# Performance work log

Measured on AMD Instinct MI355X. Metric: run time of the kernel, lower is better.

## Reference

```python
import jax, jax.numpy as jnp
import numpy as np

EMBED_DIM = 768
NUM_HEADS = 12
HEAD_DIM = EMBED_DIM // NUM_HEADS
SCALE = HEAD_DIM ** -0.5


def setup_inputs() -> dict:
    key = jax.random.key(0)
    k1, k2, k3, k4, k5 = jax.random.split(key, 5)
    B, T = 8, 1024
    hidden_states = jax.random.normal(k1, (B, T, EMBED_DIM), dtype=jnp.float32)
    init = 0.02
    qkv_w = jax.random.normal(k2, (EMBED_DIM, 3 * EMBED_DIM), dtype=jnp.float32) * init
    qkv_b = jnp.zeros((3 * EMBED_DIM,), dtype=jnp.float32)
    proj_w = jax.random.normal(k3, (EMBED_DIM, EMBED_DIM), dtype=jnp.float32) * init
    proj_b = jnp.zeros((EMBED_DIM,), dtype=jnp.float32)
    return {
        "hidden_states": hidden_states,
        "qkv_w": qkv_w,
        "qkv_b": qkv_b,
        "proj_w": proj_w,
        "proj_b": proj_b,
    }


def reference(hidden_states, qkv_w, qkv_b, proj_w, proj_b):
    B, T, C = hidden_states.shape
    # fused QKV projection
    mixed = hidden_states @ qkv_w + qkv_b            # [B, T, 3C]
    mixed = mixed.reshape(B, T, 3, NUM_HEADS, HEAD_DIM)
    mixed = jnp.transpose(mixed, (2, 0, 3, 1, 4))    # [3, B, H, T, D]
    q, k, v = mixed[0], mixed[1], mixed[2]
    # scaled dot-product attention (dropout is identity in eval)
    scores = jnp.einsum("bhqd,bhkd->bhqk", q, k) * SCALE
    probs = jax.nn.softmax(scores, axis=-1)
    ctx = jnp.einsum("bhqk,bhkd->bhqd", probs, v)    # [B, H, T, D]
    ctx = jnp.transpose(ctx, (0, 2, 1, 3)).reshape(B, T, C)
    out = ctx @ proj_w + proj_b
    return out
```

## Files before the change

kernel.cpp:

```cpp
#include <hip/hip_runtime.h>

#define EMBED 768
#define NHEAD 12
#define HDIM 64
#define BATCH 8
#define SEQ 1024
#define ROWS (BATCH*SEQ)
#define QKVN (3*EMBED)
#define ATTN_SCALE 0.125f

typedef short s16x8 __attribute__((ext_vector_type(8)));
typedef short s16x4 __attribute__((ext_vector_type(4)));
typedef float f32x4 __attribute__((ext_vector_type(4)));

__device__ __forceinline__ float bf2f(unsigned short u) {
    union { unsigned int i; float f; } v; v.i = ((unsigned int)u) << 16; return v.f;
}
__device__ __forceinline__ unsigned short f2bf(float f) {
    unsigned int i = __builtin_bit_cast(unsigned int, f);
    i += 0x7FFFu + ((i >> 16) & 1u);
    return (unsigned short)(i >> 16);
}

__device__ __forceinline__ void async16(short* lds, const unsigned short* g) {
    __builtin_amdgcn_global_load_lds(
        (const __attribute__((address_space(1))) unsigned int*)g,
        (__attribute__((address_space(3))) unsigned int*)lds,
        16, 0, 0);
}

__device__ __forceinline__ f32x4 mfma16(s16x4 a, s16x4 b, f32x4 c) {
#if __has_builtin(__builtin_amdgcn_mfma_f32_16x16x16bf16_1k)
    return __builtin_amdgcn_mfma_f32_16x16x16bf16_1k(a, b, c, 0, 0, 0);
#else
    asm volatile("v_mfma_f32_16x16x16_bf16 %0, %1, %2, %0" : "+v"(c) : "v"(a), "v"(b));
    return c;
#endif
}

__global__ __launch_bounds__(256) void prep_k(
    const float* __restrict__ qkv_w, unsigned short* __restrict__ WqkvT,
    const float* __restrict__ proj_w, unsigned short* __restrict__ WprojT,
    const float* __restrict__ hidden, unsigned short* __restrict__ hiddenBf)
{
    __shared__ float tile[64][65];
    int blk = blockIdx.x;
    int t = threadIdx.x;
    if (blk < 576) {
        const float* in; unsigned short* outp; int K, N, tx, ty;
        if (blk < 432) { in = qkv_w; outp = WqkvT; K = EMBED; N = QKVN; tx = blk % 36; ty = blk / 36; }
        else { int b2 = blk - 432; in = proj_w; outp = WprojT; K = EMBED; N = EMBED; tx = b2 % 12; ty = b2 / 12; }
        int n0 = tx * 64, k0 = ty * 64;
        int c = t & 63, r0 = t >> 6;
        #pragma unroll
        for (int i = 0; i < 16; i++) {
            int r = r0 * 16 + i;
            tile[r][c] = in[(long long)(k0 + r) * N + n0 + c];
        }
        __syncthreads();
        #pragma unroll
        for (int i = 0; i < 16; i++) {
            int nr = r0 * 16 + i;
            outp[(long long)(n0 + nr) * K + k0 + c] = f2bf(tile[c][nr]);
        }
    } else {
        int tid = (blk - 576) * 256 + t;
        int base = tid * 8;
        float4 f0 = *(const float4*)&hidden[base];
        float4 f1 = *(const float4*)&hidden[base + 4];
        s16x8 a;
        a[0] = (short)f2bf(f0.x); a[1] = (short)f2bf(f0.y);
        a[2] = (short)f2bf(f0.z); a[3] = (short)f2bf(f0.w);
        a[4] = (short)f2bf(f1.x); a[5] = (short)f2bf(f1.y);
        a[6] = (short)f2bf(f1.z); a[7] = (short)f2bf(f1.w);
        *(s16x8*)&hiddenBf[base] = a;
    }
}

template <int OUT_F32>
__global__ __launch_bounds__(256) void gemm128(
    const unsigned short* __restrict__ A,
    const unsigned short* __restrict__ Bt,
    const float* __restrict__ bias,
    void* __restrict__ Cv,
    int M, int N, int K)
{
    __shared__ short As[128 * 32];
    __shared__ short Bs[128 * 32];
    int t = threadIdx.x, lane = t & 63, w = t >> 6;
    int quad = lane >> 4, low = lane & 15;
    int m0 = blockIdx.x * 128, n0 = blockIdx.y * 128;
    int wm = (w & 1) * 64, wn = (w >> 1) * 64;

    int ci0 = w * 128 + lane;
    int r0 = ci0 >> 2, c0 = (ci0 & 3) ^ ((r0 >> 1) & 3);
    int ci1 = ci0 + 64;
    int r1 = ci1 >> 2, c1 = (ci1 & 3) ^ ((r1 >> 1) & 3);
    const unsigned short* pa0 = A + (long long)(m0 + r0) * K + c0 * 8;
    const unsigned short* pa1 = A + (long long)(m0 + r1) * K + c1 * 8;
    const unsigned short* pb0 = Bt + (long long)(n0 + r0) * K + c0 * 8;
    const unsigned short* pb1 = Bt + (long long)(n0 + r1) * K + c1 * 8;
    short* la0 = As + (w * 128) * 8;
    short* la1 = As + (w * 128 + 64) * 8;
    short* lb0 = Bs + (w * 128) * 8;
    short* lb1 = Bs + (w * 128 + 64) * 8;

    f32x4 acc[4][4] = {};
    for (int k0 = 0; k0 < K; k0 += 32) {
        __syncthreads();
        async16(la0, pa0 + k0);
        async16(la1, pa1 + k0);
        async16(lb0, pb0 + k0);
        async16(lb1, pb1 + k0);
        __syncthreads();
        s16x8 af[4], bfr[4];
        #pragma unroll
        for (int i = 0; i < 4; i++) {
            int ra = wm + i * 16 + low;
            af[i] = *(const s16x8*)&As[ra * 32 + ((quad ^ ((ra >> 1) & 3)) * 8)];
            int rb = wn + i * 16 + low;
            bfr[i] = *(const s16x8*)&Bs[rb * 32 + ((quad ^ ((rb >> 1) & 3)) * 8)];
        }
        #pragma unroll
        for (int i = 0; i < 4; i++)
            #pragma unroll
            for (int j = 0; j < 4; j++)
                acc[i][j] = __builtin_amdgcn_mfma_f32_16x16x32_bf16(af[i], bfr[j], acc[i][j], 0, 0, 0);
    }
    #pragma unroll
    for (int i = 0; i < 4; i++)
        #pragma unroll
        for (int j = 0; j < 4; j++)
            #pragma unroll
            for (int r = 0; r < 4; r++) {
                int m = m0 + wm + i * 16 + quad * 4 + r;
                int n = n0 + wn + j * 16 + low;
                float v = acc[i][j][r] + bias[n];
                if (OUT_F32) ((float*)Cv)[(long long)m * N + n] = v;
                else ((unsigned short*)Cv)[(long long)m * N + n] = f2bf(v);
            }
}

__global__ __launch_bounds__(256) void attn_k(
    const unsigned short* __restrict__ mixed,
    unsigned short* __restrict__ ctx)
{
    __shared__ short Ks[64 * 64];
    __shared__ short Vt[64 * 68];
    int blk = blockIdx.x;
    int bh = blk % 96;
    int qc = blk / 96;
    int b = bh / NHEAD, h = bh - b * NHEAD;
    int t = threadIdx.x;
    int lane = t & 63, w = t >> 6;
    int quad = lane >> 4, low = lane & 15;
    long long rowbase = (long long)b * SEQ;
    int q0 = qc * 128 + w * 32;
    int hoff = h * HDIM;

    s16x8 qf[2][2];
    #pragma unroll
    for (int qh = 0; qh < 2; qh++) {
        long long r = (rowbase + q0 + qh * 16 + low) * QKVN + hoff;
        qf[qh][0] = *(const s16x8*)&mixed[r + quad * 8];
        qf[qh][1] = *(const s16x8*)&mixed[r + 32 + quad * 8];
    }

    int s0 = w * 128 + lane;
    int kr0 = s0 >> 3, kc0 = s0 & 7;
    int kg = kc0 ^ (kr0 & 7);
    const unsigned short* pk0 = mixed + (rowbase + kr0) * QKVN + EMBED + hoff + kg * 8;
    const unsigned short* pk1 = mixed + (rowbase + kr0 + 8) * QKVN + EMBED + hoff + kg * 8;
    short* lk0 = Ks + (w * 128) * 8;
    short* lk1 = Ks + (w * 128 + 64) * 8;

    int dblk = t & 15, rq = t >> 4;
    const unsigned short* pv = mixed + (rowbase + rq * 4) * QKVN + 2 * EMBED + hoff + dblk * 4;

    f32x4 o[2][4] = {};
    float lsum[2] = {0.f, 0.f};

    for (int kv0 = 0; kv0 < SEQ; kv0 += 64) {
        long long koff = (long long)kv0 * QKVN;
        __syncthreads();
        async16(lk0, pk0 + koff);
        async16(lk1, pk1 + koff);
        s16x4 v0 = *(const s16x4*)&pv[koff];
        s16x4 v1 = *(const s16x4*)&pv[koff + QKVN];
        s16x4 v2 = *(const s16x4*)&pv[koff + 2 * QKVN];
        s16x4 v3 = *(const s16x4*)&pv[koff + 3 * QKVN];
        #pragma unroll
        for (int k = 0; k < 4; k++) {
            s16x4 wv;
            wv[0] = v0[k]; wv[1] = v1[k]; wv[2] = v2[k]; wv[3] = v3[k];
            *(s16x4*)&Vt[(dblk * 4 + k) * 68 + rq * 4] = wv;
        }
        __syncthreads();

        f32x4 sT[2][4] = {};
        __builtin_amdgcn_s_setprio(1);
        #pragma unroll
        for (int n = 0; n < 4; n++) {
            int rr = n * 16 + low;
            int key = low & 7;
            s16x8 kf0 = *(const s16x8*)&Ks[rr * 64 + ((quad ^ key) * 8)];
            s16x8 kf1 = *(const s16x8*)&Ks[rr * 64 + (((quad + 4) ^ key) * 8)];
            sT[0][n] = __builtin_amdgcn_mfma_f32_16x16x32_bf16(kf0, qf[0][0], sT[0][n], 0, 0, 0);
            sT[0][n] = __builtin_amdgcn_mfma_f32_16x16x32_bf16(kf1, qf[0][1], sT[0][n], 0, 0, 0);
            sT[1][n] = __builtin_amdgcn_mfma_f32_16x16x32_bf16(kf0, qf[1][0], sT[1][n], 0, 0, 0);
            sT[1][n] = __builtin_amdgcn_mfma_f32_16x16x32_bf16(kf1, qf[1][1], sT[1][n], 0, 0, 0);
        }
        __builtin_amdgcn_s_setprio(0);

        s16x4 pf[2][4];
        #pragma unroll
        for (int qh = 0; qh < 2; qh++)
            #pragma unroll
            for (int n = 0; n < 4; n++) {
                float e0 = __expf(sT[qh][n][0] * ATTN_SCALE);
                float e1 = __expf(sT[qh][n][1] * ATTN_SCALE);
                float e2 = __expf(sT[qh][n][2] * ATTN_SCALE);
                float e3 = __expf(sT[qh][n][3] * ATTN_SCALE);
                lsum[qh] += (e0 + e1) + (e2 + e3);
                unsigned int w0, w1;
                asm("v_cvt_pk_bf16_f32 %0, %1, %2" : "=v"(w0) : "v"(e0), "v"(e1));
                asm("v_cvt_pk_bf16_f32 %0, %1, %2" : "=v"(w1) : "v"(e2), "v"(e3));
                union { unsigned int u[2]; s16x4 v; } pu;
                pu.u[0] = w0; pu.u[1] = w1;
                pf[qh][n] = pu.v;
            }

        __builtin_amdgcn_s_setprio(1);
        #pragma unroll
        for (int nt = 0; nt < 4; nt++) {
            int drow = nt * 16 + low;
            #pragma unroll
            for (int n = 0; n < 4; n++) {
                s16x4 vf = *(const s16x4*)&Vt[drow * 68 + n * 16 + quad * 4];
                o[0][nt] = mfma16(pf[0][n], vf, o[0][nt]);
                o[1][nt] = mfma16(pf[1][n], vf, o[1][nt]);
            }
        }
        __builtin_amdgcn_s_setprio(0);
    }

    #pragma unroll
    for (int qh = 0; qh < 2; qh++) {
        lsum[qh] += __shfl_xor(lsum[qh], 16, 64);
        lsum[qh] += __shfl_xor(lsum[qh], 32, 64);
    }
    #pragma unroll
    for (int qh = 0; qh < 2; qh++)
        #pragma unroll
        for (int r = 0; r < 4; r++) {
            float inv = 1.0f / __shfl(lsum[qh], quad * 4 + r, 64);
            int q = q0 + qh * 16 + quad * 4 + r;
            #pragma unroll
            for (int nt = 0; nt < 4; nt++)
                ctx[(rowbase + q) * EMBED + hoff + nt * 16 + low] =
                    f2bf(o[qh][nt][r] * inv);
        }
}

extern "C" void kernel_launch(void* const* d_in, const int* in_sizes, int n_in,
                              void* d_out, int out_size, void* d_ws, size_t ws_size,
                              hipStream_t stream) {
    const float* hidden = (const float*)d_in[0];
    const float* qkv_w  = (const float*)d_in[1];
    const float* qkv_b  = (const float*)d_in[2];
    const float* proj_w = (const float*)d_in[3];
    const float* proj_b = (const float*)d_in[4];
    float* out = (float*)d_out;

    char* ws = (char*)d_ws;
    unsigned short* hiddenBf = (unsigned short*)ws;
    unsigned short* ctx      = (unsigned short*)ws;
    unsigned short* WqkvT    = (unsigned short*)(ws + 12582912);
    unsigned short* WprojT   = (unsigned short*)(ws + 16121856);
    unsigned short* mixed    = (unsigned short*)(ws + 17301504);

    prep_k<<<dim3(3648), 256, 0, stream>>>(qkv_w, WqkvT, proj_w, WprojT, hidden, hiddenBf);
    gemm128<0><<<dim3(ROWS / 128, QKVN / 128), 256, 0, stream>>>(
        hiddenBf, WqkvT, qkv_b, mixed, ROWS, QKVN, EMBED);
    attn_k<<<dim3(96 * 8), 256, 0, stream>>>(mixed, ctx);
    gemm128<1><<<dim3(ROWS / 128, EMBED / 128), 256, 0, stream>>>(
        ctx, WprojT, proj_b, out, ROWS, EMBED, EMBED);
}
```

Baseline: 198.5 us.

## Double-buffer K/V tiles in attention and fold softmax scale into Q for exp2

After: 202.0 us. No clear change (+1.8%).

```diff
diff --git a/kernel.cpp b/kernel.cpp
--- a/kernel.cpp
+++ b/kernel.cpp
@@ -8,6 +8,7 @@
 #define ROWS (BATCH*SEQ)
 #define QKVN (3*EMBED)
 #define ATTN_SCALE 0.125f
+#define QSCALE 0.18033688f
 
 typedef short s16x8 __attribute__((ext_vector_type(8)));
 typedef short s16x4 __attribute__((ext_vector_type(4)));
@@ -35,6 +36,16 @@
 #else
     asm volatile("v_mfma_f32_16x16x16_bf16 %0, %1, %2, %0" : "+v"(c) : "v"(a), "v"(b));
     return c;
+#endif
+}
+
+__device__ __forceinline__ float fast_exp2(float x) {
+#if __has_builtin(__builtin_amdgcn_exp2f)
+    return __builtin_amdgcn_exp2f(x);
+#else
+    float r;
+    asm("v_exp_f32 %0, %1" : "=v"(r) : "v"(x));
+    return r;
 #endif
 }
 
@@ -77,7 +88,7 @@
     }
 }
 
-template <int OUT_F32>
+template <int OUT_F32, int SCALEQ>
 __global__ __launch_bounds__(256) void gemm128(
     const unsigned short* __restrict__ A,
     const unsigned short* __restrict__ Bt,
@@ -136,6 +147,7 @@
                 int m = m0 + wm + i * 16 + quad * 4 + r;
                 int n = n0 + wn + j * 16 + low;
                 float v = acc[i][j][r] + bias[n];
+                if (SCALEQ && n < EMBED) v *= QSCALE;
                 if (OUT_F32) ((float*)Cv)[(long long)m * N + n] = v;
                 else ((unsigned short*)Cv)[(long long)m * N + n] = f2bf(v);
             }
@@ -145,8 +157,8 @@
     const unsigned short* __restrict__ mixed,
     unsigned short* __restrict__ ctx)
 {
-    __shared__ short Ks[64 * 64];
-    __shared__ short Vt[64 * 68];
+    __shared__ short Ks[2][64 * 64];
+    __shared__ short Vt[2][64 * 68];
     int blk = blockIdx.x;
     int bh = blk % 96;
     int qc = blk / 96;
@@ -171,8 +183,6 @@
     int kg = kc0 ^ (kr0 & 7);
     const unsigned short* pk0 = mixed + (rowbase + kr0) * QKVN + EMBED + hoff + kg * 8;
     const unsigned short* pk1 = mixed + (rowbase + kr0 + 8) * QKVN + EMBED + hoff + kg * 8;
-    short* lk0 = Ks + (w * 128) * 8;
-    short* lk1 = Ks + (w * 128 + 64) * 8;
 
     int dblk = t & 15, rq = t >> 4;
     const unsigned short* pv = mixed + (rowbase + rq * 4) * QKVN + 2 * EMBED + hoff + dblk * 4;
@@ -180,22 +190,39 @@
     f32x4 o[2][4] = {};
     float lsum[2] = {0.f, 0.f};
 
-    for (int kv0 = 0; kv0 < SEQ; kv0 += 64) {
-        long long koff = (long long)kv0 * QKVN;
-        __syncthreads();
-        async16(lk0, pk0 + koff);
-        async16(lk1, pk1 + koff);
-        s16x4 v0 = *(const s16x4*)&pv[koff];
-        s16x4 v1 = *(const s16x4*)&pv[koff + QKVN];
-        s16x4 v2 = *(const s16x4*)&pv[koff + 2 * QKVN];
-        s16x4 v3 = *(const s16x4*)&pv[koff + 3 * QKVN];
+    {
+        async16(&Ks[0][(w * 128) * 8], pk0);
+        async16(&Ks[0][(w * 128 + 64) * 8], pk1);
+        s16x4 v0 = *(const s16x4*)&pv[0];
+        s16x4 v1 = *(const s16x4*)&pv[QKVN];
+        s16x4 v2 = *(const s16x4*)&pv[2 * QKVN];
+        s16x4 v3 = *(const s16x4*)&pv[3 * QKVN];
         #pragma unroll
         for (int k = 0; k < 4; k++) {
             s16x4 wv;
             wv[0] = v0[k]; wv[1] = v1[k]; wv[2] = v2[k]; wv[3] = v3[k];
-            *(s16x4*)&Vt[(dblk * 4 + k) * 68 + rq * 4] = wv;
-        }
-        __syncthreads();
+            *(s16x4*)&Vt[0][(dblk * 4 + k) * 68 + rq * 4] = wv;
+        }
+    }
+    __syncthreads();
+
+    #pragma unroll 2
+    for (int it = 0; it < 16; it++) {
+        int cur = it & 1;
+        const short* ks = Ks[cur];
+        const short* vt = Vt[cur];
+        bool pf = (it + 1) < 16;
+        long long koff = (long long)(it + 1) * 64 * QKVN;
+
+        s16x4 nv0, nv1, nv2, nv3;
+        if (pf) {
+            async16(&Ks[cur ^ 1][(w * 128) * 8], pk0 + koff);
+            async16(&Ks[cur ^ 1][(w * 128 + 64) * 8], pk1 + koff);
+            nv0 = *(const s16x4*)&pv[koff];
+            nv1 = *(const s16x4*)&pv[koff + QKVN];
+            nv2 = *(const s16x4*)&pv[koff + 2 * QKVN];
+            nv3 = *(const s16x4*)&pv[koff + 3 * QKVN];
+        }
 
         f32x4 sT[2][4] = {};
         __builtin_amdgcn_s_setprio(1);
@@ -203,8 +230,8 @@
         for (int n = 0; n < 4; n++) {
             int rr = n * 16 + low;
             int key = low & 7;
-            s16x8 kf0 = *(const s16x8*)&Ks[rr * 64 + ((quad ^ key) * 8)];
-            s16x8 kf1 = *(const s16x8*)&Ks[rr * 64 + (((quad + 4) ^ key) * 8)];
+            s16x8 kf0 = *(const s16x8*)&ks[rr * 64 + ((quad ^ key) * 8)];
+            s16x8 kf1 = *(const s16x8*)&ks[rr * 64 + (((quad + 4) ^ key) * 8)];
             sT[0][n] = __builtin_amdgcn_mfma_f32_16x16x32_bf16(kf0, qf[0][0], sT[0][n], 0, 0, 0);
             sT[0][n] = __builtin_amdgcn_mfma_f32_16x16x32_bf16(kf1, qf[0][1], sT[0][n], 0, 0, 0);
             sT[1][n] = __builtin_amdgcn_mfma_f32_16x16x32_bf16(kf0, qf[1][0], sT[1][n], 0, 0, 0);
@@ -212,22 +239,22 @@
         }
         __builtin_amdgcn_s_setprio(0);
 
-        s16x4 pf[2][4];
+        s16x4 pfr[2][4];
         #pragma unroll
         for (int qh = 0; qh < 2; qh++)
             #pragma unroll
             for (int n = 0; n < 4; n++) {
-                float e0 = __expf(sT[qh][n][0] * ATTN_SCALE);
-                float e1 = __expf(sT[qh][n][1] * ATTN_SCALE);
-                float e2 = __expf(sT[qh][n][2] * ATTN_SCALE);
-                float e3 = __expf(sT[qh][n][3] * ATTN_SCALE);
+                float e0 = fast_exp2(sT[qh][n][0]);
+                float e1 = fast_exp2(sT[qh][n][1]);
+                float e2 = fast_exp2(sT[qh][n][2]);
+                float e3 = fast_exp2(sT[qh][n][3]);
                 lsum[qh] += (e0 + e1) + (e2 + e3);
                 unsigned int w0, w1;
                 asm("v_cvt_pk_bf16_f32 %0, %1, %2" : "=v"(w0) : "v"(e0), "v"(e1));
                 asm("v_cvt_pk_bf16_f32 %0, %1, %2" : "=v"(w1) : "v"(e2), "v"(e3));
                 union { unsigned int u[2]; s16x4 v; } pu;
                 pu.u[0] = w0; pu.u[1] = w1;
-                pf[qh][n] = pu.v;
+                pfr[qh][n] = pu.v;
             }
 
         __builtin_amdgcn_s_setprio(1);
@@ -236,12 +263,22 @@
             int drow = nt * 16 + low;
             #pragma unroll
             for (int n = 0; n < 4; n++) {
-                s16x4 vf = *(const s16x4*)&Vt[drow * 68 + n * 16 + quad * 4];
-                o[0][nt] = mfma16(pf[0][n], vf, o[0][nt]);
-                o[1][nt] = mfma16(pf[1][n], vf, o[1][nt]);
+                s16x4 vf = *(const s16x4*)&vt[drow * 68 + n * 16 + quad * 4];
+                o[0][nt] = mfma16(pfr[0][n], vf, o[0][nt]);
+                o[1][nt] = mfma16(pfr[1][n], vf, o[1][nt]);
             }
         }
         __builtin_amdgcn_s_setprio(0);
+
+        if (pf) {
+            #pragma unroll
+            for (int k = 0; k < 4; k++) {
+                s16x4 wv;
+                wv[0] = nv0[k]; wv[1] = nv1[k]; wv[2] = nv2[k]; wv[3] = nv3[k];
+                *(s16x4*)&Vt[cur ^ 1][(dblk * 4 + k) * 68 + rq * 4] = wv;
+            }
+        }
+        __syncthreads();
     }
 
     #pragma unroll
@@ -280,9 +317,9 @@
     unsigned short* mixed    = (unsigned short*)(ws + 17301504);
 
     prep_k<<<dim3(3648), 256, 0, stream>>>(qkv_w, WqkvT, proj_w, WprojT, hidden, hiddenBf);
-    gemm128<0><<<dim3(ROWS / 128, QKVN / 128), 256, 0, stream>>>(
+    gemm128<0, 1><<<dim3(ROWS / 128, QKVN / 128), 256, 0, stream>>>(
         hiddenBf, WqkvT, qkv_b, mixed, ROWS, QKVN, EMBED);
     attn_k<<<dim3(96 * 8), 256, 0, stream>>>(mixed, ctx);
-    gemm128<1><<<dim3(ROWS / 128, EMBED / 128), 256, 0, stream>>>(
+    gemm128<1, 0><<<dim3(ROWS / 128, EMBED / 128), 256, 0, stream>>>(
         ctx, WprojT, proj_b, out, ROWS, EMBED, EMBED);
 }
```
